# Kernel optimization log

Hardware: AMD Instinct MI355X
Metric: run time of the kernel (lower is better)

## Reference

```python
import jax, jax.numpy as jnp
import numpy as np

N_NODES = 50000
N_EDGES = 800000
IN_DIM = 256
HIDDEN = 64
HEADS1 = 4
HEADS2 = 1
N_CLASSES = 64
NEG_SLOPE = 0.2


def setup_inputs() -> dict:
    key = jax.random.key(0)
    ks = jax.random.split(key, 12)
    x = jax.random.normal(ks[0], (N_NODES, IN_DIM), dtype=jnp.float32)
    src = jax.random.randint(ks[1], (N_EDGES,), 0, N_NODES, dtype=jnp.int32)
    dst = jax.random.randint(ks[2], (N_EDGES,), 0, N_NODES, dtype=jnp.int32)
    s1 = 1.0 / np.sqrt(IN_DIM)
    s2 = 1.0 / np.sqrt(HIDDEN * HEADS1)
    W1 = jax.random.normal(ks[3], (IN_DIM, HEADS1 * HIDDEN), dtype=jnp.float32) * s1
    aL1 = jax.random.normal(ks[4], (HEADS1, HIDDEN), dtype=jnp.float32) * 0.1
    aR1 = jax.random.normal(ks[5], (HEADS1, HIDDEN), dtype=jnp.float32) * 0.1
    b1 = jnp.zeros((HEADS1 * HIDDEN,), dtype=jnp.float32)
    W2 = jax.random.normal(ks[6], (HEADS1 * HIDDEN, HEADS2 * N_CLASSES), dtype=jnp.float32) * s2
    aL2 = jax.random.normal(ks[7], (HEADS2, N_CLASSES), dtype=jnp.float32) * 0.1
    aR2 = jax.random.normal(ks[8], (HEADS2, N_CLASSES), dtype=jnp.float32) * 0.1
    b2 = jnp.zeros((HEADS2 * N_CLASSES,), dtype=jnp.float32)
    resW2 = jax.random.normal(ks[9], (HEADS1 * HIDDEN, HEADS2 * N_CLASSES), dtype=jnp.float32) * s2
    return {"x": x, "W1": W1, "aL1": aL1, "aR1": aR1, "b1": b1,
            "W2": W2, "aL2": aL2, "aR2": aR2, "b2": b2, "resW2": resW2,
            "src": src, "dst": dst}


def _gat_layer(h, W, aL, aR, b, src, dst, heads, out_dim, res_W=None, activation=None):
    n = h.shape[0]
    feat = (h @ W).reshape(n, heads, out_dim)          # [N, H, D]
    el = jnp.sum(feat * aL, axis=-1)                    # [N, H]
    er = jnp.sum(feat * aR, axis=-1)                    # [N, H]
    e = el[src] + er[dst]                               # [E, H]
    e = jnp.where(e > 0, e, NEG_SLOPE * e)              # leaky_relu
    # edge softmax over incoming edges of each destination node
    m = jax.ops.segment_max(e, dst, num_segments=n)
    ex = jnp.exp(e - m[dst])
    s = jax.ops.segment_sum(ex, dst, num_segments=n)
    sd = s[dst]
    a = ex / jnp.where(sd > 0, sd, 1.0)                 # [E, H]
    msg = feat[src] * a[:, :, None]                     # [E, H, D]
    rst = jax.ops.segment_sum(msg, dst, num_segments=n)  # [N, H, D]
    if res_W is not None:
        rst = rst + (h @ res_W).reshape(n, heads, out_dim)
    rst = rst + b.reshape(1, heads, out_dim)
    if activation is not None:
        rst = activation(rst)
    return rst


def reference(x, W1, aL1, aR1, b1, W2, aL2, aR2, b2, resW2, src, dst):
    h = _gat_layer(x, W1, aL1, aR1, b1, src, dst, HEADS1, HIDDEN,
                   res_W=None, activation=jax.nn.elu)
    h = h.reshape(N_NODES, HEADS1 * HIDDEN)             # flatten(1)
    h = _gat_layer(h, W2, aL2, aR2, b2, src, dst, HEADS2, N_CLASSES,
                   res_W=resW2, activation=None)
    return h.mean(axis=1)                               # mean over heads
```

## Files before the change

### kernel.cpp

```cpp
#include <hip/hip_runtime.h>
#include <hip/hip_bf16.h>
#include <math.h>

#define N_NODES 50000
#define N_EDGES 800000
#define IN_DIM  256
#define HID     64
#define H1      4
#define F1      256
#define NC      64
#define CHUNK   128
#define NB_SCAN 49
#define GEMM1_BLOCKS 800
#define FILL_BLOCKS  ((N_EDGES+255)/256)
#define HIST4_BLOCKS ((N_EDGES/4+255)/256)

typedef __attribute__((ext_vector_type(8))) short short8v;
typedef __attribute__((ext_vector_type(4))) float float4v;

__device__ __forceinline__ float bf2f(unsigned short u){
  union { unsigned int i; float f; } c; c.i = ((unsigned int)u) << 16; return c.f;
}


__global__ __launch_bounds__(256) void hist_prepw_kernel(
    const int* __restrict__ dst, int* __restrict__ counts,
    const float* __restrict__ W1, const float* __restrict__ W2,
    const float* __restrict__ resW2,
    __hip_bfloat16* __restrict__ W1T, __hip_bfloat16* __restrict__ B2T){
  int b = blockIdx.x;
  if (b < HIST4_BLOCKS){
    int e4 = b*256 + threadIdx.x;
    if (e4 < N_EDGES/4){
      int4 d = ((const int4*)dst)[e4];
      atomicAdd(&counts[d.x], 1);
      atomicAdd(&counts[d.y], 1);
      atomicAdd(&counts[d.z], 1);
      atomicAdd(&counts[d.w], 1);
    }
  } else {
    int i = (b - HIST4_BLOCKS)*256 + threadIdx.x;
    if (i < 256*256){
      int n = i >> 8, k = i & 255;
      W1T[n*256 + k] = __float2bfloat16(W1[k*256 + n]);
    } else if (i < 256*256 + 128*256){
      int j = i - 256*256;
      int n = j >> 8, k = j & 255;
      float v = (n < 64) ? W2[k*64 + n] : resW2[k*64 + (n - 64)];
      B2T[n*256 + k] = __float2bfloat16(v);
    }
  }
}


__global__ __launch_bounds__(1024) void scan1_kernel(const int* __restrict__ counts,
                                                     int* __restrict__ part,
                                                     int* __restrict__ bsum, int n){
  __shared__ int wsum[16];
  int b = blockIdx.x, tid = threadIdx.x;
  int i = b*1024 + tid;
  int lane = tid & 63, wid = tid >> 6;
  int x = (i < n) ? counts[i] : 0;
  #pragma unroll
  for (int off = 1; off < 64; off <<= 1){ int t = __shfl_up(x, off); if (lane >= off) x += t; }
  if (lane == 63) wsum[wid] = x;
  __syncthreads();
  if (wid == 0 && lane < 16){
    int w = wsum[lane];
    #pragma unroll
    for (int off = 1; off < 16; off <<= 1){ int t = __shfl_up(w, off); if (lane >= off) w += t; }
    wsum[lane] = w;
  }
  __syncthreads();
  int incl = x + (wid ? wsum[wid-1] : 0);
  if (i < n) part[i] = incl;
  if (tid == 1023) bsum[b] = incl;
}

__global__ __launch_bounds__(1024) void scan3_kernel(const int* __restrict__ part,
                                                     const int* __restrict__ bsum,
                                                     int* __restrict__ row_ptr,
                                                     int* __restrict__ cursor, int n){
  __shared__ int off_s;
  int b = blockIdx.x, tid = threadIdx.x;
  if (tid < 64){
    int orig = (tid < NB_SCAN) ? bsum[tid] : 0;
    int x = orig;
    #pragma unroll
    for (int o = 1; o < 64; o <<= 1){ int t = __shfl_up(x, o); if (tid >= o) x += t; }
    if (tid == b) off_s = x - orig;
  }
  __syncthreads();
  int i = b*1024 + tid;
  if (i < n){
    int v = part[i] + off_s;
    row_ptr[i+1] = v; cursor[i+1] = v;
  }
  if (i == 0){ row_ptr[0] = 0; cursor[0] = 0; }
}


template<int LAYER, bool AFP32>
__device__ __forceinline__ void gemm_body(
    const void* __restrict__ Araw,
    const __hip_bfloat16* __restrict__ BT,
    __hip_bfloat16* __restrict__ Fb,
    float* __restrict__ Res,
    float* __restrict__ el, float* __restrict__ er,
    const float* __restrict__ aL, const float* __restrict__ aR,
    int M, int bm, int bn)
{
  constexpr int K = 256;
  __shared__ __hip_bfloat16 As[128*72];
  __shared__ __hip_bfloat16 Bs[128*72];
  int tid = threadIdx.x;
  int lane = tid & 63, w = tid >> 6;
  int wr = w >> 1, wc = w & 1;
  int l15 = lane & 15, l4 = lane >> 4;

  float4v acc[4][4];
  #pragma unroll
  for (int i=0;i<4;i++)
    #pragma unroll
    for (int j=0;j<4;j++) acc[i][j] = (float4v){0.f,0.f,0.f,0.f};

  for (int kt = 0; kt < K; kt += 64){
    #pragma unroll
    for (int it = 0; it < 4; it++){
      int chunk = tid + it*256;
      int r = chunk >> 3, kc = (chunk & 7)*8;
      int arow = bm*128 + r;
      if (AFP32){
        const float* Af = (const float*)Araw;
        float4 v0 = make_float4(0,0,0,0), v1 = make_float4(0,0,0,0);
        if (arow < M){
          v0 = *(const float4*)&Af[(size_t)arow*K + kt + kc];
          v1 = *(const float4*)&Af[(size_t)arow*K + kt + kc + 4];
        }
        __hip_bfloat16 t[8] = {__float2bfloat16(v0.x),__float2bfloat16(v0.y),
                               __float2bfloat16(v0.z),__float2bfloat16(v0.w),
                               __float2bfloat16(v1.x),__float2bfloat16(v1.y),
                               __float2bfloat16(v1.z),__float2bfloat16(v1.w)};
        *(int4*)&As[r*72 + kc] = *(int4*)t;
      } else {
        const __hip_bfloat16* Ab = (const __hip_bfloat16*)Araw;
        int4 va = make_int4(0,0,0,0);
        if (arow < M) va = *(const int4*)&Ab[(size_t)arow*K + kt + kc];
        *(int4*)&As[r*72 + kc] = va;
      }
      int brow = bn*128 + r;
      int4 vb = *(const int4*)&BT[(size_t)brow*K + kt + kc];
      *(int4*)&Bs[r*72 + kc] = vb;
    }
    __syncthreads();
    short8v af[4][2], bfr[4][2];
    #pragma unroll
    for (int mi=0;mi<4;mi++)
      #pragma unroll
      for (int kf=0;kf<2;kf++)
        af[mi][kf] = *(const short8v*)&As[(wr*64 + mi*16 + l15)*72 + kf*32 + l4*8];
    #pragma unroll
    for (int ni=0;ni<4;ni++)
      #pragma unroll
      for (int kf=0;kf<2;kf++)
        bfr[ni][kf] = *(const short8v*)&Bs[(wc*64 + ni*16 + l15)*72 + kf*32 + l4*8];
    #pragma unroll
    for (int mi=0;mi<4;mi++)
      #pragma unroll
      for (int ni=0;ni<4;ni++){
        acc[mi][ni] = __builtin_amdgcn_mfma_f32_16x16x32_bf16(bfr[ni][0], af[mi][0], acc[mi][ni], 0,0,0);
        acc[mi][ni] = __builtin_amdgcn_mfma_f32_16x16x32_bf16(bfr[ni][1], af[mi][1], acc[mi][ni], 0,0,0);
      }
    __syncthreads();
  }

  if (LAYER == 1){
    int h = bn*2 + wc;
    float aLv[4][4], aRv[4][4];
    #pragma unroll
    for (int ni=0;ni<4;ni++){
      float4 a = *(const float4*)&aL[h*64 + ni*16 + l4*4];
      float4 bvv = *(const float4*)&aR[h*64 + ni*16 + l4*4];
      aLv[ni][0]=a.x; aLv[ni][1]=a.y; aLv[ni][2]=a.z; aLv[ni][3]=a.w;
      aRv[ni][0]=bvv.x; aRv[ni][1]=bvv.y; aRv[ni][2]=bvv.z; aRv[ni][3]=bvv.w;
    }
    #pragma unroll
    for (int mi=0;mi<4;mi++){
      int row = bm*128 + wr*64 + mi*16 + l15;
      float sl = 0.f, sr = 0.f;
      ushort4 packs[4];
      #pragma unroll
      for (int ni=0;ni<4;ni++){
        __hip_bfloat16 o[4];
        #pragma unroll
        for (int r=0;r<4;r++){
          float v = acc[mi][ni][r];
          sl += v*aLv[ni][r]; sr += v*aRv[ni][r];
          o[r] = __float2bfloat16(v);
        }
        packs[ni] = *(ushort4*)o;
      }
      if (row < M){
        #pragma unroll
        for (int ni=0;ni<4;ni++)
          *(ushort4*)&Fb[(size_t)row*256 + h*64 + ni*16 + l4*4] = packs[ni];
      }
      sl += __shfl_xor(sl, 16); sl += __shfl_xor(sl, 32);
      sr += __shfl_xor(sr, 16); sr += __shfl_xor(sr, 32);
      if (l4 == 0 && row < M){ el[row*4 + h] = sl; er[row*4 + h] = sr; }
    }
  } else {
    if (wc == 0){
      float aLv[4][4], aRv[4][4];
      #pragma unroll
      for (int ni=0;ni<4;ni++){
        float4 a = *(const float4*)&aL[ni*16 + l4*4];
        float4 bvv = *(const float4*)&aR[ni*16 + l4*4];
        aLv[ni][0]=a.x; aLv[ni][1]=a.y; aLv[ni][2]=a.z; aLv[ni][3]=a.w;
        aRv[ni][0]=bvv.x; aRv[ni][1]=bvv.y; aRv[ni][2]=bvv.z; aRv[ni][3]=bvv.w;
      }
      #pragma unroll
      for (int mi=0;mi<4;mi++){
        int row = bm*128 + wr*64 + mi*16 + l15;
        float sl = 0.f, sr = 0.f;
        ushort4 packs[4];
        #pragma unroll
        for (int ni=0;ni<4;ni++){
          __hip_bfloat16 o[4];
          #pragma unroll
          for (int r=0;r<4;r++){
            float v = acc[mi][ni][r];
            sl += v*aLv[ni][r]; sr += v*aRv[ni][r];
            o[r] = __float2bfloat16(v);
          }
          packs[ni] = *(ushort4*)o;
        }
        if (row < M){
          #pragma unroll
          for (int ni=0;ni<4;ni++)
            *(ushort4*)&Fb[(size_t)row*64 + ni*16 + l4*4] = packs[ni];
        }
        sl += __shfl_xor(sl, 16); sl += __shfl_xor(sl, 32);
        sr += __shfl_xor(sr, 16); sr += __shfl_xor(sr, 32);
        if (l4 == 0 && row < M){ el[row] = sl; er[row] = sr; }
      }
    } else {
      #pragma unroll
      for (int mi=0;mi<4;mi++){
        int row = bm*128 + wr*64 + mi*16 + l15;
        if (row < M){
          #pragma unroll
          for (int ni=0;ni<4;ni++){
            float4 o = make_float4(acc[mi][ni][0], acc[mi][ni][1], acc[mi][ni][2], acc[mi][ni][3]);
            *(float4*)&Res[(size_t)row*64 + ni*16 + l4*4] = o;
          }
        }
      }
    }
  }
}

__global__ __launch_bounds__(256) void gemm1_fill_kernel(
    const float* __restrict__ x, const __hip_bfloat16* __restrict__ W1T,
    __hip_bfloat16* __restrict__ featb,
    float* __restrict__ el, float* __restrict__ er,
    const float* __restrict__ aL, const float* __restrict__ aR,
    const int* __restrict__ src, const int* __restrict__ dst,
    int* __restrict__ cursor, int* __restrict__ csr_src)
{
  int id = blockIdx.x;
  if (id < GEMM1_BLOCKS){
    int bn = (id >> 3) & 1;
    int bm = (id & 7) | ((id >> 4) << 3);
    if (bm*128 >= N_NODES) return;
    gemm_body<1,true>(x, W1T, featb, nullptr, el, er, aL, aR, N_NODES, bm, bn);
  } else {
    int e = (id - GEMM1_BLOCKS)*256 + threadIdx.x;
    if (e < N_EDGES){
      int slot = atomicAdd(&cursor[dst[e]], 1);
      csr_src[slot] = src[e];
    }
  }
}

__global__ __launch_bounds__(256) void gemm2_kernel(
    const __hip_bfloat16* __restrict__ A, const __hip_bfloat16* __restrict__ BT,
    __hip_bfloat16* __restrict__ Fb, float* __restrict__ Res,
    float* __restrict__ el, float* __restrict__ er,
    const float* __restrict__ aL, const float* __restrict__ aR, int M)
{
  gemm_body<2,false>(A, BT, Fb, Res, el, er, aL, aR, M, blockIdx.x, 0);
}


__global__ __launch_bounds__(256) void agg1_kernel(const int* __restrict__ row_ptr,
                                                   const int* __restrict__ csr_src,
                                                   const float* __restrict__ el,
                                                   const float* __restrict__ er,
                                                   const __hip_bfloat16* __restrict__ featb,
                                                   const float* __restrict__ bias,
                                                   __hip_bfloat16* __restrict__ h1b, int N){
  __shared__ int   ssh[4][CHUNK];
  __shared__ float wsh[4][CHUNK][4];
  int lane = threadIdx.x & 63, wv = threadIdx.x >> 6;
  int n = blockIdx.x*4 + wv;
  if (n >= N) return;
  int rs = row_ptr[n], re = row_ptr[n+1];
  int half = lane >> 5;
  int l31 = lane & 31;
  int hl = l31 >> 3;
  float4 ern4 = *(const float4*)&er[(size_t)n*4];
  float ernv[4] = {ern4.x, ern4.y, ern4.z, ern4.w};
  float acc[8] = {0.f,0.f,0.f,0.f,0.f,0.f,0.f,0.f};
  float ssum4[4] = {0.f,0.f,0.f,0.f};

  for (int base = rs; base < re; base += CHUNK){
    int cnt = min(CHUNK, re - base);
    int padded = (cnt + 15) & ~15;
    for (int t = lane; t < padded; t += 64){
      float w4[4] = {0.f,0.f,0.f,0.f};
      int s = 0;
      if (t < cnt){
        s = csr_src[base + t];
        float4 e4 = *(const float4*)&el[(size_t)s*4];
        float ev[4] = {e4.x, e4.y, e4.z, e4.w};
        #pragma unroll
        for (int h = 0; h < 4; h++){
          float e = ev[h] + ernv[h];
          e = e > 0.f ? e : 0.2f*e;
          float ex = __expf(e);
          w4[h] = ex;
          ssum4[h] += ex;
        }
      }
      ssh[wv][t] = s;
      *(float4*)&wsh[wv][t][0] = make_float4(w4[0], w4[1], w4[2], w4[3]);
    }
    for (int jb = 0; jb < padded; jb += 16){
      int s0 = ssh[wv][jb +      half], s1 = ssh[wv][jb +  2 + half];
      int s2 = ssh[wv][jb +  4 + half], s3 = ssh[wv][jb +  6 + half];
      int s4 = ssh[wv][jb +  8 + half], s5 = ssh[wv][jb + 10 + half];
      int s6 = ssh[wv][jb + 12 + half], s7 = ssh[wv][jb + 14 + half];
      float w0 = wsh[wv][jb +      half][hl], w1 = wsh[wv][jb +  2 + half][hl];
      float w2 = wsh[wv][jb +  4 + half][hl], w3 = wsh[wv][jb +  6 + half][hl];
      float w4_ = wsh[wv][jb +  8 + half][hl], w5 = wsh[wv][jb + 10 + half][hl];
      float w6 = wsh[wv][jb + 12 + half][hl], w7 = wsh[wv][jb + 14 + half][hl];
      short8v f0 = *(const short8v*)&featb[(size_t)s0*256 + l31*8];
      short8v f1 = *(const short8v*)&featb[(size_t)s1*256 + l31*8];
      short8v f2 = *(const short8v*)&featb[(size_t)s2*256 + l31*8];
      short8v f3 = *(const short8v*)&featb[(size_t)s3*256 + l31*8];
      short8v f4 = *(const short8v*)&featb[(size_t)s4*256 + l31*8];
      short8v f5 = *(const short8v*)&featb[(size_t)s5*256 + l31*8];
      short8v f6 = *(const short8v*)&featb[(size_t)s6*256 + l31*8];
      short8v f7 = *(const short8v*)&featb[(size_t)s7*256 + l31*8];
      #pragma unroll
      for (int q = 0; q < 8; q++){
        acc[q] += w0 * bf2f((unsigned short)f0[q]);
        acc[q] += w1 * bf2f((unsigned short)f1[q]);
        acc[q] += w2 * bf2f((unsigned short)f2[q]);
        acc[q] += w3 * bf2f((unsigned short)f3[q]);
        acc[q] += w4_ * bf2f((unsigned short)f4[q]);
        acc[q] += w5 * bf2f((unsigned short)f5[q]);
        acc[q] += w6 * bf2f((unsigned short)f6[q]);
        acc[q] += w7 * bf2f((unsigned short)f7[q]);
      }
    }
  }
  #pragma unroll
  for (int off = 32; off; off >>= 1)
    #pragma unroll
    for (int h = 0; h < 4; h++) ssum4[h] += __shfl_xor(ssum4[h], off);
  #pragma unroll
  for (int q = 0; q < 8; q++) acc[q] += __shfl_xor(acc[q], 32);
  float inv = ssum4[hl] > 0.f ? 1.f/ssum4[hl] : 0.f;
  if (lane < 32){
    float4 b0 = *(const float4*)&bias[l31*8];
    float4 b1v = *(const float4*)&bias[l31*8 + 4];
    float bb[8] = {b0.x,b0.y,b0.z,b0.w,b1v.x,b1v.y,b1v.z,b1v.w};
    __hip_bfloat16 o[8];
    #pragma unroll
    for (int q = 0; q < 8; q++){
      float v = acc[q]*inv + bb[q];
      v = v > 0.f ? v : __expf(v) - 1.f;
      o[q] = __float2bfloat16(v);
    }
    *(short8v*)&h1b[(size_t)n*256 + l31*8] = *(short8v*)o;
  }
}

__global__ __launch_bounds__(256) void agg2_kernel(const int* __restrict__ row_ptr,
                                                   const int* __restrict__ csr_src,
                                                   const float* __restrict__ el,
                                                   const float* __restrict__ er,
                                                   const __hip_bfloat16* __restrict__ f2b,
                                                   const float* __restrict__ res,
                                                   const float* __restrict__ bias,
                                                   float* __restrict__ out, int N){
  __shared__ int   ssh[4][CHUNK];
  __shared__ float wsh[4][CHUNK];
  int lane = threadIdx.x & 63, wv = threadIdx.x >> 6;
  int n = blockIdx.x*4 + wv;
  if (n >= N) return;
  int rs = row_ptr[n], re = row_ptr[n+1];
  int q4 = lane >> 4;
  int l15 = lane & 15;
  float ern = er[n];
  float acc[4] = {0.f,0.f,0.f,0.f};
  float ssum = 0.f;

  for (int base = rs; base < re; base += CHUNK){
    int cnt = min(CHUNK, re - base);
    int padded = (cnt + 15) & ~15;
    for (int t = lane; t < padded; t += 64){
      float w = 0.f; int s = 0;
      if (t < cnt){
        s = csr_src[base + t];
        float e = el[s] + ern;
        e = e > 0.f ? e : 0.2f*e;
        w = __expf(e);
        ssum += w;
      }
      ssh[wv][t] = s;
      wsh[wv][t] = w;
    }
    for (int jb = 0; jb < padded; jb += 16){
      int t0 = jb + q4, t1 = jb + 4 + q4, t2 = jb + 8 + q4, t3 = jb + 12 + q4;
      int s0 = ssh[wv][t0], s1 = ssh[wv][t1], s2 = ssh[wv][t2], s3 = ssh[wv][t3];
      float w0 = wsh[wv][t0], w1 = wsh[wv][t1], w2 = wsh[wv][t2], w3 = wsh[wv][t3];
      ushort4 f0 = *(const ushort4*)&f2b[(size_t)s0*NC + l15*4];
      ushort4 f1 = *(const ushort4*)&f2b[(size_t)s1*NC + l15*4];
      ushort4 f2 = *(const ushort4*)&f2b[(size_t)s2*NC + l15*4];
      ushort4 f3 = *(const ushort4*)&f2b[(size_t)s3*NC + l15*4];
      acc[0] += w0*bf2f(f0.x) + w1*bf2f(f1.x) + w2*bf2f(f2.x) + w3*bf2f(f3.x);
      acc[1] += w0*bf2f(f0.y) + w1*bf2f(f1.y) + w2*bf2f(f2.y) + w3*bf2f(f3.y);
      acc[2] += w0*bf2f(f0.z) + w1*bf2f(f1.z) + w2*bf2f(f2.z) + w3*bf2f(f3.z);
      acc[3] += w0*bf2f(f0.w) + w1*bf2f(f1.w) + w2*bf2f(f2.w) + w3*bf2f(f3.w);
    }
  }
  #pragma unroll
  for (int off = 32; off; off >>= 1) ssum += __shfl_xor(ssum, off);
  #pragma unroll
  for (int q = 0; q < 4; q++){
    acc[q] += __shfl_xor(acc[q], 16);
    acc[q] += __shfl_xor(acc[q], 32);
  }
  float inv = ssum > 0.f ? 1.f/ssum : 0.f;
  if (lane < 16){
    float4 r4 = *(const float4*)&res[(size_t)n*NC + l15*4];
    float4 b4 = *(const float4*)&bias[l15*4];
    float4 o;
    o.x = acc[0]*inv + r4.x + b4.x;
    o.y = acc[1]*inv + r4.y + b4.y;
    o.z = acc[2]*inv + r4.z + b4.z;
    o.w = acc[3]*inv + r4.w + b4.w;
    *(float4*)&out[(size_t)n*NC + l15*4] = o;
  }
}


extern "C" void kernel_launch(void* const* d_in, const int* in_sizes, int n_in,
                              void* d_out, int out_size, void* d_ws, size_t ws_size,
                              hipStream_t stream){
  const float* x     = (const float*)d_in[0];
  const float* W1    = (const float*)d_in[1];
  const float* aL1   = (const float*)d_in[2];
  const float* aR1   = (const float*)d_in[3];
  const float* b1    = (const float*)d_in[4];
  const float* W2    = (const float*)d_in[5];
  const float* aL2   = (const float*)d_in[6];
  const float* aR2   = (const float*)d_in[7];
  const float* b2    = (const float*)d_in[8];
  const float* resW2 = (const float*)d_in[9];
  const int*   src   = (const int*)d_in[10];
  const int*   dst   = (const int*)d_in[11];
  float* out = (float*)d_out;

  char* p = (char*)d_ws;
  auto alloc = [&](size_t bytes)->void*{
    void* r = (void*)p; p += (bytes + 255) & ~(size_t)255; return r;
  };
  __hip_bfloat16* featb = (__hip_bfloat16*)alloc((size_t)N_NODES*F1*2);
  __hip_bfloat16* h1b   = (__hip_bfloat16*)alloc((size_t)N_NODES*F1*2);
  __hip_bfloat16* f2b   = (__hip_bfloat16*)alloc((size_t)N_NODES*NC*2);
  float* res   = (float*)alloc((size_t)N_NODES*NC*4);
  float* el1   = (float*)alloc((size_t)N_NODES*H1*4);
  float* er1   = (float*)alloc((size_t)N_NODES*H1*4);
  float* el2   = (float*)alloc((size_t)N_NODES*4);
  float* er2   = (float*)alloc((size_t)N_NODES*4);
  int* counts  = (int*)alloc((size_t)N_NODES*4);
  int* part    = (int*)alloc((size_t)N_NODES*4);
  int* bsum    = (int*)alloc((size_t)64*4);
  int* row_ptr = (int*)alloc((size_t)(N_NODES+1)*4);
  int* cursor  = (int*)alloc((size_t)(N_NODES+1)*4);
  int* csr_src = (int*)alloc((size_t)N_EDGES*4);
  __hip_bfloat16* W1T = (__hip_bfloat16*)alloc((size_t)256*256*2);
  __hip_bfloat16* B2T = (__hip_bfloat16*)alloc((size_t)128*256*2);

  int nb = (N_NODES + 1023)/1024;
  int prepw_blocks = (256*256 + 128*256 + 255)/256;
  hipMemsetAsync(counts, 0, (size_t)N_NODES*4, stream);
  hist_prepw_kernel<<<HIST4_BLOCKS + prepw_blocks, 256, 0, stream>>>(dst, counts,
                                                                     W1, W2, resW2, W1T, B2T);
  scan1_kernel<<<nb, 1024, 0, stream>>>(counts, part, bsum, N_NODES);
  scan3_kernel<<<nb, 1024, 0, stream>>>(part, bsum, row_ptr, cursor, N_NODES);

  gemm1_fill_kernel<<<GEMM1_BLOCKS + FILL_BLOCKS, 256, 0, stream>>>(
      x, W1T, featb, el1, er1, aL1, aR1, src, dst, cursor, csr_src);

  agg1_kernel<<<(N_NODES+3)/4, 256, 0, stream>>>(row_ptr, csr_src, el1, er1, featb, b1, h1b, N_NODES);

  gemm2_kernel<<<(N_NODES+127)/128, 256, 0, stream>>>(h1b, B2T, f2b, res,
                                                      el2, er2, aL2, aR2, N_NODES);
  agg2_kernel<<<(N_NODES+3)/4, 256, 0, stream>>>(row_ptr, csr_src, el2, er2, f2b, res, b2, out, N_NODES);
}
```

Measured before the change: 222.1 us.

## Record per-edge slot in histogram to drop fill atomics; narrow agg1 unroll

The histogram pass now keeps the return value of each atomicAdd as a per-edge slot. The CSR fill then writes to row_ptr[dst]+slot with no second round of atomics, and the cursor array and its copy in the scan are removed. This costs an extra 3.2MB eslot write and read. Separately, agg1 now gathers 4 neighbours per step with padding to 8 instead of 8 with padding to 16, which cuts wasted padded work on low-degree nodes but leaves fewer loads in flight.

Measured after the change: 187.6 us, median of 2. 15.5% less time.

```diff
diff --git a/kernel.cpp b/kernel.cpp
--- a/kernel.cpp
+++ b/kernel.cpp
@@ -24,7 +24,7 @@
 
 
 __global__ __launch_bounds__(256) void hist_prepw_kernel(
-    const int* __restrict__ dst, int* __restrict__ counts,
+    const int* __restrict__ dst, int* __restrict__ counts, int* __restrict__ eslot,
     const float* __restrict__ W1, const float* __restrict__ W2,
     const float* __restrict__ resW2,
     __hip_bfloat16* __restrict__ W1T, __hip_bfloat16* __restrict__ B2T){
@@ -33,10 +33,12 @@
     int e4 = b*256 + threadIdx.x;
     if (e4 < N_EDGES/4){
       int4 d = ((const int4*)dst)[e4];
-      atomicAdd(&counts[d.x], 1);
-      atomicAdd(&counts[d.y], 1);
-      atomicAdd(&counts[d.z], 1);
-      atomicAdd(&counts[d.w], 1);
+      int4 s;
+      s.x = atomicAdd(&counts[d.x], 1);
+      s.y = atomicAdd(&counts[d.y], 1);
+      s.z = atomicAdd(&counts[d.z], 1);
+      s.w = atomicAdd(&counts[d.w], 1);
+      ((int4*)eslot)[e4] = s;
     }
   } else {
     int i = (b - HIST4_BLOCKS)*256 + threadIdx.x;
@@ -79,8 +81,7 @@
 
 __global__ __launch_bounds__(1024) void scan3_kernel(const int* __restrict__ part,
                                                      const int* __restrict__ bsum,
-                                                     int* __restrict__ row_ptr,
-                                                     int* __restrict__ cursor, int n){
+                                                     int* __restrict__ row_ptr, int n){
   __shared__ int off_s;
   int b = blockIdx.x, tid = threadIdx.x;
   if (tid < 64){
@@ -92,11 +93,8 @@
   }
   __syncthreads();
   int i = b*1024 + tid;
-  if (i < n){
-    int v = part[i] + off_s;
-    row_ptr[i+1] = v; cursor[i+1] = v;
-  }
-  if (i == 0){ row_ptr[0] = 0; cursor[0] = 0; }
+  if (i < n) row_ptr[i+1] = part[i] + off_s;
+  if (i == 0) row_ptr[0] = 0;
 }
 
 
@@ -266,7 +264,8 @@
     float* __restrict__ el, float* __restrict__ er,
     const float* __restrict__ aL, const float* __restrict__ aR,
     const int* __restrict__ src, const int* __restrict__ dst,
-    int* __restrict__ cursor, int* __restrict__ csr_src)
+    const int* __restrict__ row_ptr, const int* __restrict__ eslot,
+    int* __restrict__ csr_src)
 {
   int id = blockIdx.x;
   if (id < GEMM1_BLOCKS){
@@ -277,8 +276,8 @@
   } else {
     int e = (id - GEMM1_BLOCKS)*256 + threadIdx.x;
     if (e < N_EDGES){
-      int slot = atomicAdd(&cursor[dst[e]], 1);
-      csr_src[slot] = src[e];
+      int d = dst[e];
+      csr_src[row_ptr[d] + eslot[e]] = src[e];
     }
   }
 }
@@ -316,7 +315,7 @@
 
   for (int base = rs; base < re; base += CHUNK){
     int cnt = min(CHUNK, re - base);
-    int padded = (cnt + 15) & ~15;
+    int padded = (cnt + 7) & ~7;
     for (int t = lane; t < padded; t += 64){
       float w4[4] = {0.f,0.f,0.f,0.f};
       int s = 0;
@@ -336,33 +335,21 @@
       ssh[wv][t] = s;
       *(float4*)&wsh[wv][t][0] = make_float4(w4[0], w4[1], w4[2], w4[3]);
     }
-    for (int jb = 0; jb < padded; jb += 16){
-      int s0 = ssh[wv][jb +      half], s1 = ssh[wv][jb +  2 + half];
-      int s2 = ssh[wv][jb +  4 + half], s3 = ssh[wv][jb +  6 + half];
-      int s4 = ssh[wv][jb +  8 + half], s5 = ssh[wv][jb + 10 + half];
-      int s6 = ssh[wv][jb + 12 + half], s7 = ssh[wv][jb + 14 + half];
-      float w0 = wsh[wv][jb +      half][hl], w1 = wsh[wv][jb +  2 + half][hl];
-      float w2 = wsh[wv][jb +  4 + half][hl], w3 = wsh[wv][jb +  6 + half][hl];
-      float w4_ = wsh[wv][jb +  8 + half][hl], w5 = wsh[wv][jb + 10 + half][hl];
-      float w6 = wsh[wv][jb + 12 + half][hl], w7 = wsh[wv][jb + 14 + half][hl];
+    for (int jb = 0; jb < padded; jb += 8){
+      int t0 = jb + half, t1 = jb + 2 + half, t2 = jb + 4 + half, t3 = jb + 6 + half;
+      int s0 = ssh[wv][t0], s1 = ssh[wv][t1], s2 = ssh[wv][t2], s3 = ssh[wv][t3];
+      float w0 = wsh[wv][t0][hl], w1 = wsh[wv][t1][hl];
+      float w2 = wsh[wv][t2][hl], w3 = wsh[wv][t3][hl];
       short8v f0 = *(const short8v*)&featb[(size_t)s0*256 + l31*8];
       short8v f1 = *(const short8v*)&featb[(size_t)s1*256 + l31*8];
       short8v f2 = *(const short8v*)&featb[(size_t)s2*256 + l31*8];
       short8v f3 = *(const short8v*)&featb[(size_t)s3*256 + l31*8];
-      short8v f4 = *(const short8v*)&featb[(size_t)s4*256 + l31*8];
-      short8v f5 = *(const short8v*)&featb[(size_t)s5*256 + l31*8];
-      short8v f6 = *(const short8v*)&featb[(size_t)s6*256 + l31*8];
-      short8v f7 = *(const short8v*)&featb[(size_t)s7*256 + l31*8];
       #pragma unroll
       for (int q = 0; q < 8; q++){
         acc[q] += w0 * bf2f((unsigned short)f0[q]);
         acc[q] += w1 * bf2f((unsigned short)f1[q]);
         acc[q] += w2 * bf2f((unsigned short)f2[q]);
         acc[q] += w3 * bf2f((unsigned short)f3[q]);
-        acc[q] += w4_ * bf2f((unsigned short)f4[q]);
-        acc[q] += w5 * bf2f((unsigned short)f5[q]);
-        acc[q] += w6 * bf2f((unsigned short)f6[q]);
-        acc[q] += w7 * bf2f((unsigned short)f7[q]);
       }
     }
   }
@@ -491,7 +478,7 @@
   int* part    = (int*)alloc((size_t)N_NODES*4);
   int* bsum    = (int*)alloc((size_t)64*4);
   int* row_ptr = (int*)alloc((size_t)(N_NODES+1)*4);
-  int* cursor  = (int*)alloc((size_t)(N_NODES+1)*4);
+  int* eslot   = (int*)alloc((size_t)N_EDGES*4);
   int* csr_src = (int*)alloc((size_t)N_EDGES*4);
   __hip_bfloat16* W1T = (__hip_bfloat16*)alloc((size_t)256*256*2);
   __hip_bfloat16* B2T = (__hip_bfloat16*)alloc((size_t)128*256*2);
@@ -499,13 +486,13 @@
   int nb = (N_NODES + 1023)/1024;
   int prepw_blocks = (256*256 + 128*256 + 255)/256;
   hipMemsetAsync(counts, 0, (size_t)N_NODES*4, stream);
-  hist_prepw_kernel<<<HIST4_BLOCKS + prepw_blocks, 256, 0, stream>>>(dst, counts,
+  hist_prepw_kernel<<<HIST4_BLOCKS + prepw_blocks, 256, 0, stream>>>(dst, counts, eslot,
                                                                      W1, W2, resW2, W1T, B2T);
   scan1_kernel<<<nb, 1024, 0, stream>>>(counts, part, bsum, N_NODES);
-  scan3_kernel<<<nb, 1024, 0, stream>>>(part, bsum, row_ptr, cursor, N_NODES);
+  scan3_kernel<<<nb, 1024, 0, stream>>>(part, bsum, row_ptr, N_NODES);
 
   gemm1_fill_kernel<<<GEMM1_BLOCKS + FILL_BLOCKS, 256, 0, stream>>>(
-      x, W1T, featb, el1, er1, aL1, aR1, src, dst, cursor, csr_src);
+      x, W1T, featb, el1, er1, aL1, aR1, src, dst, row_ptr, eslot, csr_src);
 
   agg1_kernel<<<(N_NODES+3)/4, 256, 0, stream>>>(row_ptr, csr_src, el1, er1, featb, b1, h1b, N_NODES);
 
```
